# Optimization experiments

Hardware: AMD Instinct MI355X
Metric: run time of the kernel (lower is better)

Reference implementation:

```python
import jax, jax.numpy as jnp
import numpy as np

B, S, HID = 1, 2048, 1024
NH, NKV, HD = 16, 4, 64
SCALING = 0.125  # attention_multiplier = 1/sqrt(head_dim)
ROPE_THETA = 10000.0
NEG_MIN = jnp.finfo(jnp.float32).min


def rotate_half(x):
    x1, x2 = jnp.split(x, 2, axis=-1)
    return jnp.concatenate([-x2, x1], axis=-1)


def setup_inputs() -> dict:
    key = jax.random.key(0)
    ks = jax.random.split(key, 6)
    hidden_states = jax.random.normal(ks[0], (B, S, HID), dtype=jnp.float32)
    # RoPE tables: [1, 1, S, HD]
    inv_freq = 1.0 / (ROPE_THETA ** (np.arange(0, HD, 2, dtype=np.float32) / HD))
    t = np.arange(S, dtype=np.float32)
    freqs = np.outer(t, inv_freq)                      # [S, HD/2]
    emb = np.concatenate([freqs, freqs], axis=-1)      # [S, HD]
    cos = jnp.asarray(np.cos(emb))[None, None]
    sin = jnp.asarray(np.sin(emb))[None, None]
    attention_mask = jnp.ones((B, S), dtype=bool)
    sc = 0.02
    Wq = jax.random.normal(ks[1], (HID, NH * HD), dtype=jnp.float32) * sc
    Wk = jax.random.normal(ks[2], (HID, NKV * HD), dtype=jnp.float32) * sc
    Wv = jax.random.normal(ks[3], (HID, NKV * HD), dtype=jnp.float32) * sc
    Wo = jax.random.normal(ks[4], (NH * HD, HID), dtype=jnp.float32) * sc
    return {"hidden_states": hidden_states, "cos": cos, "sin": sin,
            "attention_mask": attention_mask, "Wq": Wq, "Wk": Wk, "Wv": Wv, "Wo": Wo}


def reference(hidden_states, cos, sin, attention_mask, Wq, Wk, Wv, Wo):
    b, s, _ = hidden_states.shape
    # projections -> [B, H, S, D]
    q = (hidden_states @ Wq).reshape(b, s, NH, HD).transpose(0, 2, 1, 3)
    k = (hidden_states @ Wk).reshape(b, s, NKV, HD).transpose(0, 2, 1, 3)
    v = (hidden_states @ Wv).reshape(b, s, NKV, HD).transpose(0, 2, 1, 3)
    # RoPE (full head_dim rotation; cos/sin broadcast over batch/heads)
    q = q * cos + rotate_half(q) * sin
    k = k * cos + rotate_half(k) * sin
    # repeat_kv: expand kv heads to match query heads
    n_rep = NH // NKV
    k = jnp.repeat(k, n_rep, axis=1)
    v = jnp.repeat(v, n_rep, axis=1)
    # scores: [B, H, Sq, Sk]
    attn = jnp.einsum('bhqd,bhkd->bhqk', q, k) * SCALING
    mask = attention_mask[:, None, None, :].astype(attn.dtype)  # bool padding mask
    attn = attn + (1.0 - mask) * NEG_MIN
    attn = jax.nn.softmax(attn.astype(jnp.float32), axis=-1).astype(q.dtype)
    out = jnp.einsum('bhqk,bhkd->bhqd', attn, v)
    out = out.transpose(0, 2, 1, 3).reshape(b, s, NH * HD)
    return out @ Wo
```

## Files before the change

kernel.cpp:

```cpp
#include <hip/hip_runtime.h>
#include <stdint.h>

typedef __attribute__((ext_vector_type(8))) short short8;
typedef __attribute__((ext_vector_type(4))) short short4v;
typedef __attribute__((ext_vector_type(4))) float floatx4;
typedef __attribute__((ext_vector_type(2))) unsigned int uint2v;

#define AS1 __attribute__((address_space(1)))
#define AS3 __attribute__((address_space(3)))

__device__ __forceinline__ void async16(const void* g, void* l) {
  __builtin_amdgcn_global_load_lds((const AS1 unsigned int*)g, (AS3 unsigned int*)l, 16, 0, 0);
}

__device__ __forceinline__ short f2bf(float f) {
  unsigned u = __float_as_uint(f);
  u = (u + 0x7FFF + ((u >> 16) & 1)) >> 16;
  return (short)u;
}

__device__ __forceinline__ unsigned f2bf2(float lo, float hi) {
  return __builtin_amdgcn_perm(__float_as_uint(hi) + 0x8000u,
                               __float_as_uint(lo) + 0x8000u, 0x07060302u);
}

__device__ __forceinline__ void stage_sw(const short* src, int stride,
                                         short* tile, int cb, int lane) {
  int i = cb + lane;
  int r = i >> 3, j = i & 7;
  async16(src + (size_t)r * stride + ((j ^ (r & 7)) * 8), tile + cb * 8);
}
__device__ __forceinline__ int sw(int row, int c8) {
  return row * 64 + ((c8 ^ (row & 7)) * 8);
}

__global__ void k_prep(const float* __restrict__ X, const float* __restrict__ Wq,
                       const float* __restrict__ Wk, const float* __restrict__ Wv,
                       const float* __restrict__ Wo, short* __restrict__ Xb,
                       short* __restrict__ Wqkvt, short* __restrict__ Wot) {
  int b = blockIdx.x, tid = threadIdx.x;
  if (b < 2048) {
    int i = b * 1024 + tid * 4;
    floatx4 v = *(const floatx4*)(X + i);
    short4v o;
    o.x = f2bf(v.x); o.y = f2bf(v.y); o.z = f2bf(v.z); o.w = f2bf(v.w);
    *(short4v*)(Xb + i) = o;
    return;
  }
  const float* src; short* dst; int N, brel, rowoff;
  if (b < 3072)      { src = Wq; dst = Wqkvt; N = 1024; brel = b - 2048; rowoff = 0; }
  else if (b < 3328) { src = Wk; dst = Wqkvt; N = 256;  brel = b - 3072; rowoff = 1024; }
  else if (b < 3584) { src = Wv; dst = Wqkvt; N = 256;  brel = b - 3328; rowoff = 1280; }
  else               { src = Wo; dst = Wot;   N = 1024; brel = b - 3584; rowoff = 0; }
  __shared__ short t[32][33];
  int nt = N >> 5;
  int n0 = (brel % nt) * 32, k0 = (brel / nt) * 32;
  int tx = tid & 31, ty = tid >> 5;
#pragma unroll
  for (int i = 0; i < 4; i++)
    t[ty + 8 * i][tx] = f2bf(src[(size_t)(k0 + ty + 8 * i) * N + n0 + tx]);
  __syncthreads();
#pragma unroll
  for (int i = 0; i < 4; i++)
    dst[(size_t)(rowoff + n0 + ty + 8 * i) * 1024 + k0 + tx] = t[tx][ty + 8 * i];
}

__global__ __launch_bounds__(256) void k_gemmqkv(const short* __restrict__ A,
                                                 const short* __restrict__ Bt,
                                                 short* __restrict__ Qb,
                                                 short* __restrict__ Kb,
                                                 short* __restrict__ Vtb,
                                                 const float* __restrict__ cosp,
                                                 const float* __restrict__ sinp,
                                                 float qscale) {
  int tid = threadIdx.x;
  int w = tid >> 6, lane = tid & 63, quad = lane >> 4, l16 = lane & 15;
  __shared__ short As[2][4096];
  __shared__ short Bs[2][8192];
  const int K = 1024;
  const short* Ag = A + (size_t)(blockIdx.y * 64) * K;
  const short* Bg = Bt + (size_t)(blockIdx.x * 128) * K;
  int hw = w & 1;
  int dlo = (w >> 1) * 16 + l16;
  floatx4 acc[4][2] = {};
#pragma unroll
  for (int t = 0; t < 2; t++) stage_sw(Ag, K, As[0], (w * 2 + t) * 64, lane);
#pragma unroll
  for (int t = 0; t < 4; t++) stage_sw(Bg, K, Bs[0], (w * 4 + t) * 64, lane);
  for (int kt = 0; kt < 16; kt++) {
    __syncthreads();
    int cur = kt & 1, nxt = cur ^ 1;
    if (kt + 1 < 16) {
#pragma unroll
      for (int t = 0; t < 2; t++) stage_sw(Ag + (kt + 1) * 64, K, As[nxt], (w * 2 + t) * 64, lane);
#pragma unroll
      for (int t = 0; t < 4; t++) stage_sw(Bg + (kt + 1) * 64, K, Bs[nxt], (w * 4 + t) * 64, lane);
    }
#pragma unroll
    for (int ks = 0; ks < 2; ks++) {
      short8 af[4], bfr[2];
#pragma unroll
      for (int i = 0; i < 4; i++)
        af[i] = *(const short8*)&As[cur][sw(i * 16 + l16, ks * 4 + quad)];
#pragma unroll
      for (int j = 0; j < 2; j++)
        bfr[j] = *(const short8*)&Bs[cur][sw(hw * 64 + j * 32 + (w >> 1) * 16 + l16, ks * 4 + quad)];
#pragma unroll
      for (int i = 0; i < 4; i++)
#pragma unroll
        for (int j = 0; j < 2; j++)
          acc[i][j] = __builtin_amdgcn_mfma_f32_16x16x32_bf16(af[i], bfr[j], acc[i][j], 0, 0, 0);
    }
  }
  int bx = blockIdx.x, by = blockIdx.y;
  if (bx < 10) {
    short* dst; float scale;
    if (bx < 8) { dst = Qb + (size_t)(bx * 2 + hw) * 2048 * 64; scale = qscale; }
    else        { dst = Kb + (size_t)((bx - 8) * 2 + hw) * 2048 * 64; scale = 1.0f; }
#pragma unroll
    for (int i = 0; i < 4; i++)
#pragma unroll
      for (int r = 0; r < 4; r++) {
        int s = by * 64 + i * 16 + quad * 4 + r;
        float c = cosp[s * 64 + dlo], sn = sinp[s * 64 + dlo];
        float v0 = acc[i][0][r], v1 = acc[i][1][r];
        dst[(size_t)s * 64 + dlo]      = f2bf((v0 * c - v1 * sn) * scale);
        dst[(size_t)s * 64 + 32 + dlo] = f2bf((v1 * c + v0 * sn) * scale);
      }
  } else {
    short* dst = Vtb + (size_t)((bx - 10) * 2 + hw) * 64 * 2048;
#pragma unroll
    for (int j = 0; j < 2; j++) {
      int d = j * 32 + dlo;
#pragma unroll
      for (int i = 0; i < 4; i++) {
        short4v pk;
#pragma unroll
        for (int r = 0; r < 4; r++) pk[r] = f2bf(acc[i][j][r]);
        *(short4v*)&dst[(size_t)d * 2048 + by * 64 + i * 16 + quad * 4] = pk;
      }
    }
  }
}

__global__ __launch_bounds__(256) void k_gemm(const short* __restrict__ A,
                                              const short* __restrict__ Bt,
                                              float* __restrict__ C,
                                              int M, int N, int K) {
  int tid = threadIdx.x;
  int w = tid >> 6, lane = tid & 63, quad = lane >> 4, l16 = lane & 15;
  __shared__ short As[2][4096];
  __shared__ short Bs[2][8192];
  const short* Ag = A + (size_t)(blockIdx.y * 64) * K;
  const short* Bg = Bt + (size_t)(blockIdx.x * 128) * K;
  floatx4 acc[4][2] = {};
  int kiters = K >> 6;
#pragma unroll
  for (int t = 0; t < 2; t++) stage_sw(Ag, K, As[0], (w * 2 + t) * 64, lane);
#pragma unroll
  for (int t = 0; t < 4; t++) stage_sw(Bg, K, Bs[0], (w * 4 + t) * 64, lane);
  for (int kt = 0; kt < kiters; kt++) {
    __syncthreads();
    int cur = kt & 1, nxt = cur ^ 1;
    if (kt + 1 < kiters) {
#pragma unroll
      for (int t = 0; t < 2; t++) stage_sw(Ag + (kt + 1) * 64, K, As[nxt], (w * 2 + t) * 64, lane);
#pragma unroll
      for (int t = 0; t < 4; t++) stage_sw(Bg + (kt + 1) * 64, K, Bs[nxt], (w * 4 + t) * 64, lane);
    }
#pragma unroll
    for (int ks = 0; ks < 2; ks++) {
      short8 af[4], bfr[2];
#pragma unroll
      for (int i = 0; i < 4; i++)
        af[i] = *(const short8*)&As[cur][sw(i * 16 + l16, ks * 4 + quad)];
#pragma unroll
      for (int j = 0; j < 2; j++)
        bfr[j] = *(const short8*)&Bs[cur][sw(w * 32 + j * 16 + l16, ks * 4 + quad)];
#pragma unroll
      for (int i = 0; i < 4; i++)
#pragma unroll
        for (int j = 0; j < 2; j++)
          acc[i][j] = __builtin_amdgcn_mfma_f32_16x16x32_bf16(af[i], bfr[j], acc[i][j], 0, 0, 0);
    }
  }
#pragma unroll
  for (int i = 0; i < 4; i++)
#pragma unroll
    for (int j = 0; j < 2; j++)
#pragma unroll
      for (int r = 0; r < 4; r++) {
        int row = blockIdx.y * 64 + i * 16 + quad * 4 + r;
        int col = blockIdx.x * 128 + w * 32 + j * 16 + l16;
        C[(size_t)row * N + col] = acc[i][j][r];
      }
}

__global__ __launch_bounds__(256) void k_attn(const short* __restrict__ Qb,
                                              const short* __restrict__ Kb,
                                              const short* __restrict__ Vt,
                                              float* __restrict__ Opart,
                                              float* __restrict__ lpart) {
  int qt = blockIdx.x;
  int h = blockIdx.y;
  int sp = blockIdx.z;
  int kvh = h >> 2;
  int tid = threadIdx.x, w = tid >> 6, lane = tid & 63, quad = lane >> 4, l16 = lane & 15;
  __shared__ short Ks[2][4096];
  __shared__ short Ps[4][32 * 72];
  const short* Qg = Qb + ((size_t)h * 2048 + qt * 128 + w * 32) * 64;
  const short* Kg0 = Kb + ((size_t)kvh * 2048 + sp * 512) * 64;
  const short* Vg = Vt + (size_t)kvh * 64 * 2048 + sp * 512;
  short8 qf[2][2];
#pragma unroll
  for (int q2 = 0; q2 < 2; q2++)
#pragma unroll
    for (int ks = 0; ks < 2; ks++)
      qf[q2][ks] = *(const short8*)(Qg + (q2 * 16 + l16) * 64 + ks * 32 + quad * 8);
#pragma unroll
  for (int t = 0; t < 2; t++) stage_sw(Kg0, 64, Ks[0], (w * 2 + t) * 64, lane);
  floatx4 accO[2][4] = {};
  float lsum[2] = {0.f, 0.f};
  short* myPs = Ps[w];
  for (int kt = 0; kt < 8; kt++) {
    __syncthreads();
    short8 vf[2][4];
#pragma unroll
    for (int dt = 0; dt < 4; dt++)
      vf[0][dt] = *(const short8*)(Vg + (size_t)(dt * 16 + l16) * 2048 + kt * 64 + quad * 8);
    if (kt + 1 < 8) {
      int nb = (kt + 1) & 1;
#pragma unroll
      for (int t = 0; t < 2; t++)
        stage_sw(Kg0 + (kt + 1) * 4096, 64, Ks[nb], (w * 2 + t) * 64, lane);
    }
    int cbuf = kt & 1;
    floatx4 accS[2][4] = {};
#pragma unroll
    for (int ks = 0; ks < 2; ks++)
#pragma unroll
      for (int mt = 0; mt < 4; mt++) {
        short8 af = *(const short8*)&Ks[cbuf][sw(mt * 16 + l16, ks * 4 + quad)];
#pragma unroll
        for (int q2 = 0; q2 < 2; q2++)
          accS[q2][mt] = __builtin_amdgcn_mfma_f32_16x16x32_bf16(af, qf[q2][ks], accS[q2][mt], 0, 0, 0);
      }
#pragma unroll
    for (int dt = 0; dt < 4; dt++)
      vf[1][dt] = *(const short8*)(Vg + (size_t)(dt * 16 + l16) * 2048 + kt * 64 + 32 + quad * 8);
#pragma unroll
    for (int q2 = 0; q2 < 2; q2++)
#pragma unroll
      for (int mt = 0; mt < 4; mt++) {
        float p0 = __builtin_amdgcn_exp2f(accS[q2][mt][0]);
        float p1 = __builtin_amdgcn_exp2f(accS[q2][mt][1]);
        float p2 = __builtin_amdgcn_exp2f(accS[q2][mt][2]);
        float p3 = __builtin_amdgcn_exp2f(accS[q2][mt][3]);
        lsum[q2] += (p0 + p1) + (p2 + p3);
        uint2v pk;
        pk.x = f2bf2(p0, p1);
        pk.y = f2bf2(p2, p3);
        *(uint2v*)&myPs[(q2 * 16 + l16) * 72 + mt * 16 + quad * 4] = pk;
      }
    asm volatile("s_waitcnt lgkmcnt(0)" ::: "memory");
#pragma unroll
    for (int ks = 0; ks < 2; ks++) {
      short8 pf[2];
#pragma unroll
      for (int q2 = 0; q2 < 2; q2++)
        pf[q2] = *(const short8*)&myPs[(q2 * 16 + l16) * 72 + ks * 32 + quad * 8];
#pragma unroll
      for (int dt = 0; dt < 4; dt++)
#pragma unroll
        for (int q2 = 0; q2 < 2; q2++)
          accO[q2][dt] = __builtin_amdgcn_mfma_f32_16x16x32_bf16(pf[q2], vf[ks][dt], accO[q2][dt], 0, 0, 0);
    }
  }
  float* Op = Opart + (size_t)sp * 2048 * 1024;
#pragma unroll
  for (int q2 = 0; q2 < 2; q2++) {
    float ls = lsum[q2];
    ls += __shfl_xor(ls, 16);
    ls += __shfl_xor(ls, 32);
    if (lane < 16)
      lpart[(size_t)sp * 16 * 2048 + h * 2048 + qt * 128 + w * 32 + q2 * 16 + lane] = ls;
#pragma unroll
    for (int dt = 0; dt < 4; dt++)
#pragma unroll
      for (int r = 0; r < 4; r++) {
        int srow = qt * 128 + w * 32 + q2 * 16 + quad * 4 + r;
        int col = h * 64 + dt * 16 + l16;
        Op[(size_t)srow * 1024 + col] = accO[q2][dt][r];
      }
  }
}

__global__ void k_comb(const float* __restrict__ Opart, const float* __restrict__ lpart,
                       short* __restrict__ AOb) {
  int idx = (blockIdx.x * 256 + threadIdx.x) * 4;
  int s = idx >> 10, h = (idx & 1023) >> 6;
  float l = 0.f;
#pragma unroll
  for (int sp = 0; sp < 4; sp++) l += lpart[sp * 16 * 2048 + h * 2048 + s];
  float inv = 1.0f / l;
  floatx4 a = *(const floatx4*)(Opart + idx);
#pragma unroll
  for (int sp = 1; sp < 4; sp++) {
    floatx4 b = *(const floatx4*)(Opart + (size_t)sp * 2048 * 1024 + idx);
    a.x += b.x; a.y += b.y; a.z += b.z; a.w += b.w;
  }
  uint2v pk;
  pk.x = f2bf2(a.x * inv, a.y * inv);
  pk.y = f2bf2(a.z * inv, a.w * inv);
  *(uint2v*)&AOb[idx] = pk;
}

extern "C" void kernel_launch(void* const* d_in, const int* in_sizes, int n_in,
                              void* d_out, int out_size, void* d_ws, size_t ws_size,
                              hipStream_t stream) {
  const float* X    = (const float*)d_in[0];
  const float* cosp = (const float*)d_in[1];
  const float* sinp = (const float*)d_in[2];
  const float* Wq = (const float*)d_in[4];
  const float* Wk = (const float*)d_in[5];
  const float* Wv = (const float*)d_in[6];
  const float* Wo = (const float*)d_in[7];
  float* out = (float*)d_out;

  short* Xb    = (short*)d_ws;
  short* Wqkvt = Xb + 2097152;
  short* Wot   = Wqkvt + 1572864;
  short* Qb2   = Wot + 1048576;
  short* Kb2   = Qb2 + 2097152;
  short* Vtb   = Kb2 + 524288;
  short* AOb   = Vtb + 524288;
  float* Opart = (float*)(AOb + 2097152);
  float* lpart = Opart + 4 * 2097152;

  const float QSCALE = 0.125f * 1.44269504088896340736f;

  k_prep<<<4608, 256, 0, stream>>>(X, Wq, Wk, Wv, Wo, Xb, Wqkvt, Wot);
  k_gemmqkv<<<dim3(12, 32), 256, 0, stream>>>(Xb, Wqkvt, Qb2, Kb2, Vtb, cosp, sinp, QSCALE);
  k_attn<<<dim3(16, 16, 4), 256, 0, stream>>>(Qb2, Kb2, Vtb, Opart, lpart);
  k_comb<<<2048, 256, 0, stream>>>(Opart, lpart, AOb);
  k_gemm<<<dim3(8, 32), 256, 0, stream>>>(AOb, Wot, out, 2048, 1024, 1024);
}
```

Before: 169.4 us.

## Compute softmax row sums via MFMA with ones vector; use hardware bf16 pack

The per-row softmax denominator is now accumulated with an extra MFMA against a ones-column B operand on the same bf16 P fragments, replacing the VALU adds and cross-lane shuffles. Float-to-bf16 packing uses the hardware cvt_pk_bf16_f32 builtin when available. All V fragment loads are issued up front, and the attention kernel gets an occupancy hint of 4 blocks per CU. The row sum now comes from bf16-rounded probabilities, matching what multiplies V, and the extra accL registers plus the occupancy bound may add register pressure or spills.

After: 165.1 us. -2.5%, faster.

```diff
diff --git a/kernel.cpp b/kernel.cpp
--- a/kernel.cpp
+++ b/kernel.cpp
@@ -19,10 +19,18 @@
   return (short)u;
 }
 
-__device__ __forceinline__ unsigned f2bf2(float lo, float hi) {
+#if __has_builtin(__builtin_amdgcn_cvt_pk_bf16_f32)
+typedef __bf16 bf16x2 __attribute__((ext_vector_type(2)));
+__device__ __forceinline__ unsigned pack2(float lo, float hi) {
+  bf16x2 t = __builtin_amdgcn_cvt_pk_bf16_f32(lo, hi);
+  return *(unsigned*)&t;
+}
+#else
+__device__ __forceinline__ unsigned pack2(float lo, float hi) {
   return __builtin_amdgcn_perm(__float_as_uint(hi) + 0x8000u,
                                __float_as_uint(lo) + 0x8000u, 0x07060302u);
 }
+#endif
 
 __device__ __forceinline__ void stage_sw(const short* src, int stride,
                                          short* tile, int cb, int lane) {
@@ -196,11 +204,11 @@
       }
 }
 
-__global__ __launch_bounds__(256) void k_attn(const short* __restrict__ Qb,
-                                              const short* __restrict__ Kb,
-                                              const short* __restrict__ Vt,
-                                              float* __restrict__ Opart,
-                                              float* __restrict__ lpart) {
+__global__ __launch_bounds__(256, 4) void k_attn(const short* __restrict__ Qb,
+                                                 const short* __restrict__ Kb,
+                                                 const short* __restrict__ Vt,
+                                                 float* __restrict__ Opart,
+                                                 float* __restrict__ lpart) {
   int qt = blockIdx.x;
   int h = blockIdx.y;
   int sp = blockIdx.z;
@@ -219,15 +227,23 @@
       qf[q2][ks] = *(const short8*)(Qg + (q2 * 16 + l16) * 64 + ks * 32 + quad * 8);
 #pragma unroll
   for (int t = 0; t < 2; t++) stage_sw(Kg0, 64, Ks[0], (w * 2 + t) * 64, lane);
+  short8 vf_ones;
+  {
+    short one = (short)0x3F80;
+#pragma unroll
+    for (int j = 0; j < 8; j++) vf_ones[j] = (l16 == 0) ? one : (short)0;
+  }
   floatx4 accO[2][4] = {};
-  float lsum[2] = {0.f, 0.f};
+  floatx4 accL[2] = {};
   short* myPs = Ps[w];
   for (int kt = 0; kt < 8; kt++) {
     __syncthreads();
     short8 vf[2][4];
 #pragma unroll
-    for (int dt = 0; dt < 4; dt++)
-      vf[0][dt] = *(const short8*)(Vg + (size_t)(dt * 16 + l16) * 2048 + kt * 64 + quad * 8);
+    for (int ks = 0; ks < 2; ks++)
+#pragma unroll
+      for (int dt = 0; dt < 4; dt++)
+        vf[ks][dt] = *(const short8*)(Vg + (size_t)(dt * 16 + l16) * 2048 + kt * 64 + ks * 32 + quad * 8);
     if (kt + 1 < 8) {
       int nb = (kt + 1) & 1;
 #pragma unroll
@@ -245,9 +261,6 @@
         for (int q2 = 0; q2 < 2; q2++)
           accS[q2][mt] = __builtin_amdgcn_mfma_f32_16x16x32_bf16(af, qf[q2][ks], accS[q2][mt], 0, 0, 0);
       }
-#pragma unroll
-    for (int dt = 0; dt < 4; dt++)
-      vf[1][dt] = *(const short8*)(Vg + (size_t)(dt * 16 + l16) * 2048 + kt * 64 + 32 + quad * 8);
 #pragma unroll
     for (int q2 = 0; q2 < 2; q2++)
 #pragma unroll
@@ -256,10 +269,9 @@
         float p1 = __builtin_amdgcn_exp2f(accS[q2][mt][1]);
         float p2 = __builtin_amdgcn_exp2f(accS[q2][mt][2]);
         float p3 = __builtin_amdgcn_exp2f(accS[q2][mt][3]);
-        lsum[q2] += (p0 + p1) + (p2 + p3);
         uint2v pk;
-        pk.x = f2bf2(p0, p1);
-        pk.y = f2bf2(p2, p3);
+        pk.x = pack2(p0, p1);
+        pk.y = pack2(p2, p3);
         *(uint2v*)&myPs[(q2 * 16 + l16) * 72 + mt * 16 + quad * 4] = pk;
       }
     asm volatile("s_waitcnt lgkmcnt(0)" ::: "memory");
@@ -270,6 +282,9 @@
       for (int q2 = 0; q2 < 2; q2++)
         pf[q2] = *(const short8*)&myPs[(q2 * 16 + l16) * 72 + ks * 32 + quad * 8];
 #pragma unroll
+      for (int q2 = 0; q2 < 2; q2++)
+        accL[q2] = __builtin_amdgcn_mfma_f32_16x16x32_bf16(pf[q2], vf_ones, accL[q2], 0, 0, 0);
+#pragma unroll
       for (int dt = 0; dt < 4; dt++)
 #pragma unroll
         for (int q2 = 0; q2 < 2; q2++)
@@ -279,11 +294,11 @@
   float* Op = Opart + (size_t)sp * 2048 * 1024;
 #pragma unroll
   for (int q2 = 0; q2 < 2; q2++) {
-    float ls = lsum[q2];
-    ls += __shfl_xor(ls, 16);
-    ls += __shfl_xor(ls, 32);
-    if (lane < 16)
-      lpart[(size_t)sp * 16 * 2048 + h * 2048 + qt * 128 + w * 32 + q2 * 16 + lane] = ls;
+    if (l16 == 0) {
+#pragma unroll
+      for (int r = 0; r < 4; r++)
+        lpart[(size_t)sp * 16 * 2048 + h * 2048 + qt * 128 + w * 32 + q2 * 16 + quad * 4 + r] = accL[q2][r];
+    }
 #pragma unroll
     for (int dt = 0; dt < 4; dt++)
 #pragma unroll
@@ -310,8 +325,8 @@
     a.x += b.x; a.y += b.y; a.z += b.z; a.w += b.w;
   }
   uint2v pk;
-  pk.x = f2bf2(a.x * inv, a.y * inv);
-  pk.y = f2bf2(a.z * inv, a.w * inv);
+  pk.x = pack2(a.x * inv, a.y * inv);
+  pk.y = pack2(a.z * inv, a.w * inv);
   *(uint2v*)&AOb[idx] = pk;
 }
 
```
